# Optimization experiments

Hardware: AMD Instinct MI355X
Metric: run time of the kernel (lower is better)

The kernel has to match this reference:

```python
import jax, jax.numpy as jnp
import numpy as np

VOCAB = 50000
EMBED_DIM = 1024
HALF = EMBED_DIM // 2
BATCH, SEQ = 32, 2048


def setup_inputs() -> dict:
    key = jax.random.key(0)
    ks = jax.random.split(key, 7)
    token_ids = jax.random.randint(ks[0], (BATCH, SEQ), 0, VOCAB)
    token_table = jax.random.normal(ks[1], (VOCAB, HALF), dtype=jnp.float32)
    op_table = jax.random.normal(ks[2], (10, HALF), dtype=jnp.float32)
    var_table = jax.random.normal(ks[3], (10, HALF), dtype=jnp.float32)
    const_table = jax.random.normal(ks[4], (10, HALF), dtype=jnp.float32)
    struct_table = jax.random.normal(ks[5], (10, HALF), dtype=jnp.float32)
    special_table = jax.random.normal(ks[6], (VOCAB - 40, HALF), dtype=jnp.float32)
    return {
        "token_ids": token_ids,
        "token_table": token_table,
        "op_table": op_table,
        "var_table": var_table,
        "const_table": const_table,
        "struct_table": struct_table,
        "special_table": special_table,
    }


def reference(token_ids, token_table, op_table, var_table, const_table,
              struct_table, special_table):
    # Token-path embedding: [B, S, HALF]
    token_embeds = token_table[token_ids]
    # The per-category tables stacked along rows align exactly with token ids:
    # category start offsets (0,10,20,30,40) equal the cumulative row offsets,
    # so the masked bucketize+gather collapses to one gather from the concat.
    cat_table = jnp.concatenate(
        [op_table, var_table, const_table, struct_table, special_table], axis=0)
    category_embeds = cat_table[token_ids]  # [B, S, HALF]
    return jnp.concatenate([token_embeds, category_embeds], axis=-1)
```

## Files before the change

kernel.cpp:

```cpp
#include <hip/hip_runtime.h>


typedef float f32x4 __attribute__((ext_vector_type(4)));

#define HALF_DIM 512
#define V4_PER_HALF (HALF_DIM / 4)

__global__ __launch_bounds__(256) void compemb_kernel(
    const int* __restrict__ ids,
    const f32x4* __restrict__ tok,
    const f32x4* __restrict__ op_t,
    const f32x4* __restrict__ var_t,
    const f32x4* __restrict__ cst_t,
    const f32x4* __restrict__ str_t,
    const f32x4* __restrict__ spc_t,
    f32x4* __restrict__ out,
    int n_tokens)
{
    const int token = blockIdx.x;
    if (token >= n_tokens) return;

    const int id = ids[token];
    const int t  = threadIdx.x;
    const int e  = t & (V4_PER_HALF - 1);

    const f32x4* src;
    long long row;
    if (t < V4_PER_HALF) {
        src = tok;  row = id;
    } else {
        if (id < 10)      { src = op_t;  row = id; }
        else if (id < 20) { src = var_t; row = id - 10; }
        else if (id < 30) { src = cst_t; row = id - 20; }
        else if (id < 40) { src = str_t; row = id - 30; }
        else              { src = spc_t; row = id - 40; }
    }

    const f32x4 v = src[row * V4_PER_HALF + e];
    __builtin_nontemporal_store(v, &out[(long long)token * 256 + t]);
}

extern "C" void kernel_launch(void* const* d_in, const int* in_sizes, int n_in,
                              void* d_out, int out_size, void* d_ws, size_t ws_size,
                              hipStream_t stream) {
    const int*   ids   = (const int*)  d_in[0];
    const f32x4* tok   = (const f32x4*)d_in[1];
    const f32x4* op_t  = (const f32x4*)d_in[2];
    const f32x4* var_t = (const f32x4*)d_in[3];
    const f32x4* cst_t = (const f32x4*)d_in[4];
    const f32x4* str_t = (const f32x4*)d_in[5];
    const f32x4* spc_t = (const f32x4*)d_in[6];
    f32x4* out = (f32x4*)d_out;

    const int n_tokens = in_sizes[0];
    compemb_kernel<<<n_tokens, 256, 0, stream>>>(
        ids, tok, op_t, var_t, cst_t, str_t, spc_t, out, n_tokens);
}
```

Baseline: 79.74 us.

## Bucket-sort tokens by id range before gathering to improve table cache locality

Adds a histogram, prefix-scan and scatter pass that groups token indices into buckets of 256 ids, then has the gather kernel process tokens in that bucketed order. The aim is for blocks running at the same time to read nearby table rows, so the 100 MB token and special tables get better L2/MALL reuse. In exchange it adds four small kernel launches with global atomics on 65K tokens, and output writes become scattered rows rather than sequential. The bucket count of 196 is hard-coded for a vocabulary of 50000.

```diff
diff --git a/kernel.cpp b/kernel.cpp
--- a/kernel.cpp
+++ b/kernel.cpp
@@ -3,10 +3,50 @@
 
 typedef float f32x4 __attribute__((ext_vector_type(4)));
 
-#define HALF_DIM 512
-#define V4_PER_HALF (HALF_DIM / 4)
+#define V4_PER_HALF 128
+#define BUCKET_SHIFT 8
+#define NB 196
+
+
+__global__ __launch_bounds__(256) void k_zero(int* __restrict__ hist) {
+    if (threadIdx.x < NB) hist[threadIdx.x] = 0;
+}
+
+__global__ __launch_bounds__(256) void k_hist(const int* __restrict__ ids,
+                                              int* __restrict__ hist, int n) {
+    int i = blockIdx.x * 256 + threadIdx.x;
+    if (i < n) atomicAdd(&hist[ids[i] >> BUCKET_SHIFT], 1);
+}
+
+__global__ __launch_bounds__(256) void k_scan(const int* __restrict__ hist,
+                                              int* __restrict__ offs) {
+    __shared__ int s[256];
+    int t = threadIdx.x;
+    int v = (t < NB) ? hist[t] : 0;
+    s[t] = v;
+    __syncthreads();
+    for (int d = 1; d < 256; d <<= 1) {
+        int x = (t >= d) ? s[t - d] : 0;
+        __syncthreads();
+        s[t] += x;
+        __syncthreads();
+    }
+    if (t < NB) offs[t] = s[t] - v;
+}
+
+__global__ __launch_bounds__(256) void k_scatter(const int* __restrict__ ids,
+                                                 int* __restrict__ offs,
+                                                 int* __restrict__ perm, int n) {
+    int i = blockIdx.x * 256 + threadIdx.x;
+    if (i < n) {
+        int pos = atomicAdd(&offs[ids[i] >> BUCKET_SHIFT], 1);
+        perm[pos] = i;
+    }
+}
+
 
 __global__ __launch_bounds__(256) void compemb_kernel(
+    const int* __restrict__ perm,
     const int* __restrict__ ids,
     const f32x4* __restrict__ tok,
     const f32x4* __restrict__ op_t,
@@ -14,12 +54,9 @@
     const f32x4* __restrict__ cst_t,
     const f32x4* __restrict__ str_t,
     const f32x4* __restrict__ spc_t,
-    f32x4* __restrict__ out,
-    int n_tokens)
+    f32x4* __restrict__ out)
 {
-    const int token = blockIdx.x;
-    if (token >= n_tokens) return;
-
+    const int token = perm[blockIdx.x];
     const int id = ids[token];
     const int t  = threadIdx.x;
     const int e  = t & (V4_PER_HALF - 1);
@@ -40,6 +77,7 @@
     __builtin_nontemporal_store(v, &out[(long long)token * 256 + t]);
 }
 
+
 extern "C" void kernel_launch(void* const* d_in, const int* in_sizes, int n_in,
                               void* d_out, int out_size, void* d_ws, size_t ws_size,
                               hipStream_t stream) {
@@ -53,6 +91,16 @@
     f32x4* out = (f32x4*)d_out;
 
     const int n_tokens = in_sizes[0];
+
+    int* hist = (int*)d_ws;
+    int* offs = hist + 256;
+    int* perm = hist + 512;
+
+    const int nblk = (n_tokens + 255) / 256;
+    k_zero   <<<1,    256, 0, stream>>>(hist);
+    k_hist   <<<nblk, 256, 0, stream>>>(ids, hist, n_tokens);
+    k_scan   <<<1,    256, 0, stream>>>(hist, offs);
+    k_scatter<<<nblk, 256, 0, stream>>>(ids, offs, perm, n_tokens);
     compemb_kernel<<<n_tokens, 256, 0, stream>>>(
-        ids, tok, op_t, var_t, cst_t, str_t, spc_t, out, n_tokens);
+        perm, ids, tok, op_t, var_t, cst_t, str_t, spc_t, out);
 }
```

Result: slower. 161.0 us (+101.9%).
